# Performance work log

Measured on AMD Instinct MI355X. Metric: run time of the kernel, lower is better.

The kernel has to match this reference:

```python
import jax, jax.numpy as jnp
import numpy as np

B, SEQ, C_IN, F, K = 32, 16384, 64, 64, 9

def setup_inputs() -> dict:
    key = jax.random.key(0)
    k1, k2 = jax.random.split(key)
    x = jax.random.normal(k1, (B, SEQ, C_IN), dtype=jnp.float32)
    w = jax.random.normal(k2, (F, K, C_IN), dtype=jnp.float32) * 0.05  # mimics random_normal_initializer stddev
    b = jnp.zeros((F,), dtype=jnp.float32)
    return {"x": x, "w": w, "b": b}

def reference(x, w, b):
    # Faithful math: out[bt, t, f] = sum_{k,c} w[f,k,c] * x[bt, t+k, c] + b[f]
    # (VALID padding, stride 1). Expressed as an efficient conv instead of the
    # original unrolled loop + giant stacked intermediate.
    kernel = jnp.transpose(w, (1, 2, 0))  # [K, C_in, F] for WIO layout
    out = jax.lax.conv_general_dilated(
        x, kernel,
        window_strides=(1,),
        padding='VALID',
        dimension_numbers=('NWC', 'WIO', 'NWC'),
    )  # [B, SEQ-K+1, F]
    return out + b[None, None, :]
```

## Files before the change

### kernel.cpp

```cpp
#include <hip/hip_runtime.h>
#include <hip/hip_bf16.h>

#define T_IN   16384
#define T_OUT  16376
#define CIN    64
#define NF     64
#define KT     9
#define NB     32
#define TILE   128
#define ROWS   136
#define CGS    8
#define PLANE  (ROWS * 8)
#define NBLOCKS 512
#define TILE_ITERS 8
#define WS_SHORTS ((size_t)NB * T_IN * CIN)
#define WS_BYTES  (WS_SHORTS * 2)

typedef __bf16 bf16x8 __attribute__((ext_vector_type(8)));
typedef unsigned short u16x8 __attribute__((ext_vector_type(8)));
typedef unsigned short u16x4 __attribute__((ext_vector_type(4)));
typedef float f32x16 __attribute__((ext_vector_type(16)));

__device__ __forceinline__ unsigned short f2bf(float f) {
    unsigned u = __builtin_bit_cast(unsigned, f);
    u += 0x7FFFu + ((u >> 16) & 1u);
    return (unsigned short)(u >> 16);
}

__device__ __forceinline__ void async_load16(const unsigned short* g, unsigned short* l) {
    __builtin_amdgcn_global_load_lds(
        (const __attribute__((address_space(1))) void*)g,
        (__attribute__((address_space(3))) void*)l, 16, 0, 0);
}

__global__ __launch_bounds__(256) void convert_bf16_kernel(
    const float* __restrict__ x, unsigned short* __restrict__ ws)
{
    const int tid = blockIdx.x * 256 + threadIdx.x;
#pragma unroll
    for (int i = 0; i < 8; ++i) {
        const int idx = tid + i * 524288;
        const int bb  = idx >> 17;
        const int rem = idx & 131071;
        const int t   = rem >> 3;
        const int cg  = rem & 7;
        const float* xp = x + ((size_t)bb * T_IN + t) * CIN + cg * 8;
        const float4 v0 = *(const float4*)xp;
        const float4 v1 = *(const float4*)(xp + 4);
        u16x8 p;
        p[0] = f2bf(v0.x); p[1] = f2bf(v0.y); p[2] = f2bf(v0.z); p[3] = f2bf(v0.w);
        p[4] = f2bf(v1.x); p[5] = f2bf(v1.y); p[6] = f2bf(v1.z); p[7] = f2bf(v1.w);
        *(u16x8*)&ws[((size_t)(bb * CGS + cg) * T_IN + t) * 8] = p;
    }
}

__global__ __launch_bounds__(256, 2) void conv1d_mfma_dma_kernel(
    const unsigned short* __restrict__ xb,
    const float* __restrict__ w,
    const float* __restrict__ b,
    float* __restrict__ out)
{
    __shared__ __attribute__((aligned(16))) unsigned short ldsX[2][CGS * PLANE];

    const int tid  = threadIdx.x;
    const int lane = tid & 63;
    const int wv   = tid >> 6;
    const int half = lane >> 5;
    const int l31  = lane & 31;
    const int fh   = wv & 1;
    const int rh   = wv >> 1;
    const int rbase = rh * 64;
    const int fcol  = fh * 32 + l31;

    bf16x8 Bf[KT][4];
#pragma unroll
    for (int k = 0; k < KT; ++k) {
#pragma unroll
        for (int s = 0; s < 4; ++s) {
            const float* wp = w + (size_t)fcol * (KT * CIN) + k * CIN + s * 16 + half * 8;
            const float4 w0 = *(const float4*)(wp);
            const float4 w1 = *(const float4*)(wp + 4);
            u16x8 t;
            t[0] = f2bf(w0.x); t[1] = f2bf(w0.y); t[2] = f2bf(w0.z); t[3] = f2bf(w0.w);
            t[4] = f2bf(w1.x); t[5] = f2bf(w1.y); t[6] = f2bf(w1.z); t[7] = f2bf(w1.w);
            Bf[k][s] = __builtin_bit_cast(bf16x8, t);
        }
    }
    const float bias = b[fcol];

    const int base = blockIdx.x * TILE_ITERS;

    auto stage = [&](int g, int d) {
        const int bb = g >> 7;
        const int t0 = (g & 127) << 7;
        for (int j = wv; j < 24; j += 4) {
            const int cg = j / 3;
            const int p  = j - cg * 3;
            const int r0 = (p == 0) ? 0 : (p == 1) ? 64 : 72;
            int gr = t0 + r0 + lane;
            gr = gr < T_IN ? gr : (T_IN - 1);
            const unsigned short* gp = xb + ((size_t)(bb * CGS + cg) * T_IN + gr) * 8;
            async_load16(gp, &ldsX[d][(cg * ROWS + r0) * 8]);
        }
    };

    stage(base, 0);
    __syncthreads();

    for (int it = 0; it < TILE_ITERS; ++it) {
        const int g  = base + it;
        const int bb = g >> 7;
        const int t0 = (g & 127) << 7;
        const int c  = it & 1;
        const bool more = (it + 1 < TILE_ITERS);

        if (more) stage(g + 1, c ^ 1);

        f32x16 acc0 = {0,0,0,0,0,0,0,0,0,0,0,0,0,0,0,0};
        f32x16 acc1 = {0,0,0,0,0,0,0,0,0,0,0,0,0,0,0,0};
        const unsigned short* lx = &ldsX[c][half * PLANE + (rbase + l31) * 8];
#pragma unroll
        for (int k = 0; k < KT; ++k) {
#pragma unroll
            for (int s = 0; s < 4; ++s) {
                const int off = s * (2 * PLANE) + k * 8;
                bf16x8 a0 = *(const bf16x8*)&lx[off];
                bf16x8 a1 = *(const bf16x8*)&lx[off + 256];
                acc0 = __builtin_amdgcn_mfma_f32_32x32x16_bf16(a0, Bf[k][s], acc0, 0, 0, 0);
                acc1 = __builtin_amdgcn_mfma_f32_32x32x16_bf16(a1, Bf[k][s], acc1, 0, 0, 0);
            }
        }

#pragma unroll
        for (int m = 0; m < 2; ++m) {
            const f32x16 A = m ? acc1 : acc0;
#pragma unroll
            for (int r = 0; r < 16; ++r) {
                const int tl = rbase + m * 32 + (r & 3) + 8 * (r >> 2) + 4 * half;
                const int tg = t0 + tl;
                if (tg < T_OUT)
                    out[((size_t)bb * T_OUT + tg) * NF + fcol] = A[r] + bias;
            }
        }

        __syncthreads();
    }
}

#define LDS_STRIDE 72
__global__ __launch_bounds__(256, 2) void conv1d_fallback(
    const float* __restrict__ x, const float* __restrict__ w,
    const float* __restrict__ b, float* __restrict__ out)
{
    __shared__ __attribute__((aligned(16))) unsigned short ldsF[ROWS * LDS_STRIDE];
    const int tid  = threadIdx.x;
    const int lane = tid & 63;
    const int wv   = tid >> 6;
    const int half = lane >> 5;
    const int l31  = lane & 31;
    const int rbase = (wv >> 1) * 64;
    const int fcol  = (wv & 1) * 32 + l31;

    bf16x8 Bf[KT][4];
#pragma unroll
    for (int k = 0; k < KT; ++k) {
#pragma unroll
        for (int s = 0; s < 4; ++s) {
            const float* wp = w + (size_t)fcol * (KT * CIN) + k * CIN + s * 16 + half * 8;
            const float4 w0 = *(const float4*)(wp);
            const float4 w1 = *(const float4*)(wp + 4);
            u16x8 t;
            t[0] = f2bf(w0.x); t[1] = f2bf(w0.y); t[2] = f2bf(w0.z); t[3] = f2bf(w0.w);
            t[4] = f2bf(w1.x); t[5] = f2bf(w1.y); t[6] = f2bf(w1.z); t[7] = f2bf(w1.w);
            Bf[k][s] = __builtin_bit_cast(bf16x8, t);
        }
    }
    const float bias = b[fcol];

    for (int it = 0; it < TILE_ITERS; ++it) {
        const int g  = blockIdx.x * TILE_ITERS + it;
        const int bb = g >> 7;
        const int t0 = (g & 127) << 7;
        for (int i = tid; i < ROWS * 16; i += 256) {
            const int r  = i >> 4;
            const int cg = i & 15;
            int gr = t0 + r;
            gr = gr < (T_IN - 1) ? gr : (T_IN - 1);
            const float4 v = *(const float4*)(x + ((size_t)bb * T_IN + gr) * CIN + cg * 4);
            u16x4 p;
            p[0] = f2bf(v.x); p[1] = f2bf(v.y); p[2] = f2bf(v.z); p[3] = f2bf(v.w);
            *(u16x4*)&ldsF[r * LDS_STRIDE + cg * 4] = p;
        }
        __syncthreads();
        f32x16 acc0 = {0,0,0,0,0,0,0,0,0,0,0,0,0,0,0,0};
        f32x16 acc1 = {0,0,0,0,0,0,0,0,0,0,0,0,0,0,0,0};
        const int abase = (rbase + l31) * LDS_STRIDE + half * 8;
#pragma unroll
        for (int k = 0; k < KT; ++k) {
#pragma unroll
            for (int s = 0; s < 4; ++s) {
                const int off = abase + k * LDS_STRIDE + s * 16;
                bf16x8 a0 = *(const bf16x8*)&ldsF[off];
                bf16x8 a1 = *(const bf16x8*)&ldsF[off + 32 * LDS_STRIDE];
                acc0 = __builtin_amdgcn_mfma_f32_32x32x16_bf16(a0, Bf[k][s], acc0, 0, 0, 0);
                acc1 = __builtin_amdgcn_mfma_f32_32x32x16_bf16(a1, Bf[k][s], acc1, 0, 0, 0);
            }
        }
#pragma unroll
        for (int m = 0; m < 2; ++m) {
            const f32x16 A = m ? acc1 : acc0;
#pragma unroll
            for (int r = 0; r < 16; ++r) {
                const int tl = rbase + m * 32 + (r & 3) + 8 * (r >> 2) + 4 * half;
                const int tg = t0 + tl;
                if (tg < T_OUT)
                    out[((size_t)bb * T_OUT + tg) * NF + fcol] = A[r] + bias;
            }
        }
        __syncthreads();
    }
}

extern "C" void kernel_launch(void* const* d_in, const int* in_sizes, int n_in,
                              void* d_out, int out_size, void* d_ws, size_t ws_size,
                              hipStream_t stream) {
    const float* x = (const float*)d_in[0];
    const float* w = (const float*)d_in[1];
    const float* b = (const float*)d_in[2];
    float* out = (float*)d_out;
    if (ws_size >= WS_BYTES && d_ws != nullptr) {
        unsigned short* ws = (unsigned short*)d_ws;
        convert_bf16_kernel<<<2048, 256, 0, stream>>>(x, ws);
        conv1d_mfma_dma_kernel<<<NBLOCKS, 256, 0, stream>>>(ws, w, b, out);
    } else {
        conv1d_fallback<<<NBLOCKS, 256, 0, stream>>>(x, w, b, out);
    }
}
```

Baseline: 318.6 us.

## Stage conversion through LDS for coalesced writes and pack conv tile DMA

The bf16 conversion kernel now stages each 256-row chunk through a swizzled LDS buffer, so writes to the channel-group-planar workspace become contiguous runs instead of strided 16-byte scatters. The conv kernel's async LDS staging is repacked into 17 dense 64-lane loads that linearly cover all channel-group rows, replacing 24 loads that were partly redundant (overlapping 64/72 row offsets). The loop-end __syncthreads is replaced by an explicit vmcnt wait placed before the output stores plus a raw s_barrier, so the next tile's prefetch can overlap the MFMA work. The divide-by-136 via multiply-shift and the manual waitcnt add correctness risk if the store-side counters or the index mapping are wrong.

New measurement: 321.4 us. Within noise of the previous version (+0.9%).

```diff
diff --git a/kernel.cpp b/kernel.cpp
--- a/kernel.cpp
+++ b/kernel.cpp
@@ -10,7 +10,7 @@
 #define TILE   128
 #define ROWS   136
 #define CGS    8
-#define PLANE  (ROWS * 8)
+#define UNITS  (CGS * ROWS)
 #define NBLOCKS 512
 #define TILE_ITERS 8
 #define WS_SHORTS ((size_t)NB * T_IN * CIN)
@@ -36,21 +36,33 @@
 __global__ __launch_bounds__(256) void convert_bf16_kernel(
     const float* __restrict__ x, unsigned short* __restrict__ ws)
 {
-    const int tid = blockIdx.x * 256 + threadIdx.x;
-#pragma unroll
-    for (int i = 0; i < 8; ++i) {
-        const int idx = tid + i * 524288;
-        const int bb  = idx >> 17;
-        const int rem = idx & 131071;
-        const int t   = rem >> 3;
-        const int cg  = rem & 7;
-        const float* xp = x + ((size_t)bb * T_IN + t) * CIN + cg * 8;
+    __shared__ __attribute__((aligned(16))) unsigned short lds[256 * CGS * 8];
+    const int bb  = blockIdx.x >> 6;
+    const int t0  = (blockIdx.x & 63) << 8;
+    const int tid = threadIdx.x;
+#pragma unroll
+    for (int rep = 0; rep < 8; ++rep) {
+        const int u  = rep * 256 + tid;
+        const int t  = u >> 3;
+        const int cg = u & 7;
+        const float* xp = x + ((size_t)bb * T_IN + t0 + t) * CIN + cg * 8;
         const float4 v0 = *(const float4*)xp;
         const float4 v1 = *(const float4*)(xp + 4);
         u16x8 p;
         p[0] = f2bf(v0.x); p[1] = f2bf(v0.y); p[2] = f2bf(v0.z); p[3] = f2bf(v0.w);
         p[4] = f2bf(v1.x); p[5] = f2bf(v1.y); p[6] = f2bf(v1.z); p[7] = f2bf(v1.w);
-        *(u16x8*)&ws[((size_t)(bb * CGS + cg) * T_IN + t) * 8] = p;
+        const int cs = cg ^ (t & 7);
+        *(u16x8*)&lds[(t * CGS + cs) * 8] = p;
+    }
+    __syncthreads();
+#pragma unroll
+    for (int rep = 0; rep < 8; ++rep) {
+        const int u  = rep * 256 + tid;
+        const int cg = u >> 8;
+        const int t  = u & 255;
+        const int cs = cg ^ (t & 7);
+        const u16x8 p = *(const u16x8*)&lds[(t * CGS + cs) * 8];
+        *(u16x8*)&ws[((size_t)(bb * CGS + cg) * T_IN + t0 + t) * 8] = p;
     }
 }
 
@@ -60,7 +72,7 @@
     const float* __restrict__ b,
     float* __restrict__ out)
 {
-    __shared__ __attribute__((aligned(16))) unsigned short ldsX[2][CGS * PLANE];
+    __shared__ __attribute__((aligned(16))) unsigned short ldsX[2][UNITS * 8];
 
     const int tid  = threadIdx.x;
     const int lane = tid & 63;
@@ -93,14 +105,15 @@
     auto stage = [&](int g, int d) {
         const int bb = g >> 7;
         const int t0 = (g & 127) << 7;
-        for (int j = wv; j < 24; j += 4) {
-            const int cg = j / 3;
-            const int p  = j - cg * 3;
-            const int r0 = (p == 0) ? 0 : (p == 1) ? 64 : 72;
-            int gr = t0 + r0 + lane;
+        for (int j = wv; j < 17; j += 4) {
+            const int p  = j * 64 + lane;
+            const int q  = p >> 3;
+            const int cg = (q * 241) >> 12;
+            const int r  = p - cg * ROWS;
+            int gr = t0 + r;
             gr = gr < T_IN ? gr : (T_IN - 1);
             const unsigned short* gp = xb + ((size_t)(bb * CGS + cg) * T_IN + gr) * 8;
-            async_load16(gp, &ldsX[d][(cg * ROWS + r0) * 8]);
+            async_load16(gp, &ldsX[d][j * 512]);
         }
     };
 
@@ -118,18 +131,21 @@
 
         f32x16 acc0 = {0,0,0,0,0,0,0,0,0,0,0,0,0,0,0,0};
         f32x16 acc1 = {0,0,0,0,0,0,0,0,0,0,0,0,0,0,0,0};
-        const unsigned short* lx = &ldsX[c][half * PLANE + (rbase + l31) * 8];
+        const unsigned short* lx = &ldsX[c][(half * ROWS + rbase + l31) * 8];
 #pragma unroll
         for (int k = 0; k < KT; ++k) {
 #pragma unroll
             for (int s = 0; s < 4; ++s) {
-                const int off = s * (2 * PLANE) + k * 8;
+                const int off = s * (2 * ROWS * 8) + k * 8;
                 bf16x8 a0 = *(const bf16x8*)&lx[off];
                 bf16x8 a1 = *(const bf16x8*)&lx[off + 256];
                 acc0 = __builtin_amdgcn_mfma_f32_32x32x16_bf16(a0, Bf[k][s], acc0, 0, 0, 0);
                 acc1 = __builtin_amdgcn_mfma_f32_32x32x16_bf16(a1, Bf[k][s], acc1, 0, 0, 0);
             }
         }
+
+        asm volatile("s_waitcnt vmcnt(0)" ::: "memory");
+        __builtin_amdgcn_sched_barrier(0);
 
 #pragma unroll
         for (int m = 0; m < 2; ++m) {
@@ -143,7 +159,9 @@
             }
         }
 
-        __syncthreads();
+        __builtin_amdgcn_sched_barrier(0);
+        __builtin_amdgcn_s_barrier();
+        __builtin_amdgcn_sched_barrier(0);
     }
 }
 
```
